# Optimization experiments

Measured on AMD Instinct MI355X. Metric: run time of the kernel, lower is better.

## Reference

```python
import jax, jax.numpy as jnp
import numpy as np

IN_SIZE = 512
UNITS = 512
GRID_SIZE = 5
ORDER = 3
LO, HI = -1.0, 1.0
BATCH = 1024


def _make_grid():
    # grid: (in_size, grid_size + 2*order + 1), extended beyond grid_range by order knot spacings
    bound = HI - LO
    g = jnp.linspace(LO - ORDER * bound / GRID_SIZE,
                     HI + ORDER * bound / GRID_SIZE,
                     GRID_SIZE + 2 * ORDER + 1, dtype=jnp.float32)
    return jnp.tile(g[None, :], (IN_SIZE, 1))


def _spline_bases(x, grid):
    # Cox-de Boor recursion. x: (B, in), grid: (in, G)
    xe = x[..., None]  # (B, in, 1)
    bases = ((xe >= grid[:, :-1]) & (xe < grid[:, 1:])).astype(x.dtype)  # order-0 indicators
    for k in range(1, ORDER + 1):
        left = (xe - grid[:, :-(k + 1)]) / (grid[:, k:-1] - grid[:, :-(k + 1)]) * bases[..., :-1]
        right = (grid[:, k + 1:] - xe) / (grid[:, k + 1:] - grid[:, 1:-k]) * bases[..., 1:]
        bases = left + right
    return bases  # (B, in, grid_size + order)


def setup_inputs() -> dict:
    key = jax.random.key(0)
    k1, k2, k3 = jax.random.split(key, 3)
    x = jax.random.normal(k1, (BATCH, IN_SIZE), jnp.float32)
    spline_kernel = 0.1 * jax.random.normal(k2, (IN_SIZE, GRID_SIZE + ORDER, UNITS), jnp.float32)
    limit = float(np.sqrt(6.0 / (IN_SIZE + UNITS)))  # GlorotUniform
    scale_factor = jax.random.uniform(k3, (IN_SIZE, UNITS), jnp.float32, -limit, limit)
    bias = jnp.zeros((UNITS,), jnp.float32)
    return {"x": x, "spline_kernel": spline_kernel, "scale_factor": scale_factor, "bias": bias}


def reference(x, spline_kernel, scale_factor, bias):
    grid = _make_grid()
    bases = _spline_bases(x, grid)                              # (B, in, basis)
    spline_out = jnp.einsum('bik,iko->bio', bases, spline_kernel)  # (B, in, units)
    spline_out = spline_out + jax.nn.silu(x)[..., None]            # add basis activation per feature
    spline_out = spline_out * scale_factor[None]                   # per (in, units) scaling
    out = jnp.sum(spline_out, axis=-2) + bias                      # reduce over in_size
    return out
```

## Files before the change

kernel.cpp:

```cpp
#include <hip/hip_runtime.h>
#include <cstdint>
#include <cmath>

typedef unsigned short u16;
typedef __bf16 bf16x8 __attribute__((ext_vector_type(8)));
typedef float f32x4 __attribute__((ext_vector_type(4)));

#define B_SZ   1024
#define IN_SZ  512
#define U_SZ   512
#define KTOT   4608
#define SPLITS 16
#define KLEN   288
#define BK     32
#define KITERS 9

__device__ __forceinline__ u16 f2bf(float f) {
  __bf16 h = (__bf16)f;
  return __builtin_bit_cast(u16, h);
}

__device__ __forceinline__ void async16(const void* g, void* l) {
  __builtin_amdgcn_global_load_lds(
      (__attribute__((address_space(1))) void*)(g),
      (__attribute__((address_space(3))) void*)(l), 16u, 0, 0u);
}

__global__ void prep_w(const float* __restrict__ SK, const float* __restrict__ SF,
                       u16* __restrict__ WT) {
  __shared__ u16 tile[72 * 64];
  const int o0 = blockIdx.x * 64;
  const int i0 = blockIdx.y * 8;
  const int tid = threadIdx.x;
  const int oo = tid & 63, grp = tid >> 6;

  for (int tr = grp; tr < 72; tr += 4) {
    int i = i0 + tr / 9;
    int k = tr % 9;
    float sf = SF[(size_t)i * U_SZ + o0 + oo];
    float v  = (k < 8) ? SK[((size_t)i * 8 + k) * U_SZ + o0 + oo] * sf : sf;
    tile[tr * 64 + oo] = f2bf(v);
  }
  __syncthreads();

  const int t0 = i0 * 9;
  for (int idx = tid; idx < 72 * 64; idx += 256) {
    int ol = idx / 72;
    int c  = idx - ol * 72;
    WT[(size_t)(o0 + ol) * KTOT + t0 + c] = tile[c * 64 + ol];
  }
}

__global__ void bases_kernel(const float* __restrict__ X, u16* __restrict__ A) {
  const int gid = blockIdx.x * 256 + threadIdx.x;
  const float x = X[gid];

  const float T0 = -2.2f, H = 0.4f;
  float b0[11], b1[10], b2[9], b3[8];
#pragma unroll
  for (int j = 0; j < 11; ++j) {
    float tj  = T0 + H * j;
    float tj1 = T0 + H * (j + 1);
    b0[j] = (x >= tj && x < tj1) ? 1.0f : 0.0f;
  }
#pragma unroll
  for (int j = 0; j < 10; ++j) {
    float tj  = T0 + H * j;
    float tj2 = T0 + H * (j + 2);
    b1[j] = (x - tj) * 2.5f * b0[j] + (tj2 - x) * 2.5f * b0[j + 1];
  }
#pragma unroll
  for (int j = 0; j < 9; ++j) {
    float tj  = T0 + H * j;
    float tj3 = T0 + H * (j + 3);
    b2[j] = (x - tj) * 1.25f * b1[j] + (tj3 - x) * 1.25f * b1[j + 1];
  }
#pragma unroll
  for (int j = 0; j < 8; ++j) {
    float tj  = T0 + H * j;
    float tj4 = T0 + H * (j + 4);
    b3[j] = (x - tj) * (1.0f / 1.2f) * b2[j] + (tj4 - x) * (1.0f / 1.2f) * b2[j + 1];
  }
  float sil = x / (1.0f + expf(-x));

  u16* row = A + (size_t)gid * 9;
#pragma unroll
  for (int k = 0; k < 8; ++k) row[k] = f2bf(b3[k]);
  row[8] = f2bf(sil);
}

__global__ void __launch_bounds__(256) gemm_kan(const u16* __restrict__ A,
                                                const u16* __restrict__ WT,
                                                float* __restrict__ P) {
  __shared__ __align__(16) u16 sA[2][128 * BK];
  __shared__ __align__(16) u16 sB[2][128 * BK];

  const int t    = threadIdx.x;
  const int lane = t & 63;
  const int w    = t >> 6;
  const int wr   = w >> 1;
  const int wn   = w & 1;
  const int m0   = blockIdx.x * 128;
  const int n0   = blockIdx.y * 128;
  const int kbase = blockIdx.z * KLEN;

  const int srow = t >> 2, sc = t & 3;
  const int sg0 = (sc ^ (srow & 3)) * 8;
  const int srow1 = (t + 256) >> 2, sc1 = t & 3;
  const int sg1 = (sc1 ^ (srow1 & 3)) * 8;
  const u16* gA0 = A  + (size_t)(m0 + srow)  * KTOT + sg0;
  const u16* gA1 = A  + (size_t)(m0 + srow1) * KTOT + sg1;
  const u16* gB0 = WT + (size_t)(n0 + srow)  * KTOT + sg0;
  const u16* gB1 = WT + (size_t)(n0 + srow1) * KTOT + sg1;

  f32x4 acc[4][4];
#pragma unroll
  for (int i = 0; i < 4; ++i)
#pragma unroll
    for (int j = 0; j < 4; ++j) acc[i][j] = (f32x4)0.0f;

  auto stage = [&](int buf, int k0) {
    char* lA = (char*)(&sA[buf][0]) + t * 16;
    char* lB = (char*)(&sB[buf][0]) + t * 16;
    async16(gA0 + k0, lA);
    async16(gA1 + k0, lA + 4096);
    async16(gB0 + k0, lB);
    async16(gB1 + k0, lB + 4096);
  };

  stage(0, kbase);

  const int m = lane & 15, q = lane >> 4;
  const int qs = (q ^ (m & 3)) * 16;
  const char* fA = (const char*)(&sA[0][0]) + (wr * 64 + m) * (BK * 2) + qs;
  const char* fB = (const char*)(&sB[0][0]) + (wn * 64 + m) * (BK * 2) + qs;
  const int bufstep = 128 * BK * 2;

#pragma unroll
  for (int it = 0; it < KITERS; ++it) {
    const int cur = it & 1;
    __syncthreads();
    if (it + 1 < KITERS) stage(cur ^ 1, kbase + (it + 1) * BK);

    bf16x8 af[4], bfv[4];
#pragma unroll
    for (int tt = 0; tt < 4; ++tt)
      af[tt] = *(const bf16x8*)(fA + cur * bufstep + tt * 16 * (BK * 2));
#pragma unroll
    for (int tt = 0; tt < 4; ++tt)
      bfv[tt] = *(const bf16x8*)(fB + cur * bufstep + tt * 16 * (BK * 2));
#pragma unroll
    for (int mt = 0; mt < 4; ++mt)
#pragma unroll
      for (int nt = 0; nt < 4; ++nt)
        acc[mt][nt] = __builtin_amdgcn_mfma_f32_16x16x32_bf16(
            af[mt], bfv[nt], acc[mt][nt], 0, 0, 0);
  }

  float* Pp = P + (size_t)blockIdx.z * (B_SZ * U_SZ);
#pragma unroll
  for (int mt = 0; mt < 4; ++mt)
#pragma unroll
    for (int rr = 0; rr < 4; ++rr) {
      int row = m0 + wr * 64 + mt * 16 + q * 4 + rr;
      size_t rb = (size_t)row * U_SZ + n0 + wn * 64 + m;
#pragma unroll
      for (int nt = 0; nt < 4; ++nt) Pp[rb + nt * 16] = acc[mt][nt][rr];
    }
}

__global__ void reduce_kernel(const float* __restrict__ P,
                              const float* __restrict__ bias,
                              float* __restrict__ out) {
  const int idx = blockIdx.x * 256 + threadIdx.x;
  const f32x4* P4 = (const f32x4*)P;
  f32x4 acc = P4[idx];
#pragma unroll
  for (int s = 1; s < SPLITS; ++s) acc += P4[(size_t)s * (B_SZ * U_SZ / 4) + idx];
  acc += ((const f32x4*)bias)[idx & 127];
  ((f32x4*)out)[idx] = acc;
}

extern "C" void kernel_launch(void* const* d_in, const int* in_sizes, int n_in,
                              void* d_out, int out_size, void* d_ws, size_t ws_size,
                              hipStream_t stream) {
  const float* X    = (const float*)d_in[0];
  const float* SK   = (const float*)d_in[1];
  const float* SF   = (const float*)d_in[2];
  const float* bias = (const float*)d_in[3];

  char* ws = (char*)d_ws;
  u16*   WT = (u16*)ws;
  u16*   A  = (u16*)(ws + 4718592);
  float* P  = (float*)(ws + 4718592 + 9437184);

  hipLaunchKernelGGL(prep_w,        dim3(8, 64),    dim3(256), 0, stream, SK, SF, WT);
  hipLaunchKernelGGL(bases_kernel,  dim3(2048),     dim3(256), 0, stream, X, A);
  hipLaunchKernelGGL(gemm_kan,      dim3(8, 4, 16), dim3(256), 0, stream, A, WT, P);
  hipLaunchKernelGGL(reduce_kernel, dim3(512),      dim3(256), 0, stream, P, bias, (float*)d_out);
}
```

Before: 98.60 us.

## Merge prep kernels and replace split-K partial buffer with atomic accumulation

Combines weight prep, basis computation and bias initialization of the output into a single launch, and has the split-K GEMM add its results straight into the output with float atomics instead of writing 16 partial buffers and running a separate reduction. This removes two kernel launches and the round trip of 32 MB of partial sums. It also pads the transpose tile to cut LDS bank conflicts and stages basis writes through LDS so global stores coalesce. In exchange, summation order becomes nondeterministic and atomic contention on the output is added.

After: 107.5 us. 1.09x slower.

```diff
diff --git a/kernel.cpp b/kernel.cpp
--- a/kernel.cpp
+++ b/kernel.cpp
@@ -26,72 +26,84 @@
       (__attribute__((address_space(3))) void*)(l), 16u, 0, 0u);
 }
 
-__global__ void prep_w(const float* __restrict__ SK, const float* __restrict__ SF,
-                       u16* __restrict__ WT) {
-  __shared__ u16 tile[72 * 64];
-  const int o0 = blockIdx.x * 64;
-  const int i0 = blockIdx.y * 8;
+__global__ void __launch_bounds__(256) prep_all(const float* __restrict__ SK,
+                                                const float* __restrict__ SF,
+                                                const float* __restrict__ X,
+                                                const float* __restrict__ bias,
+                                                u16* __restrict__ WT,
+                                                u16* __restrict__ A,
+                                                float* __restrict__ out) {
+  const int bx = blockIdx.x;
   const int tid = threadIdx.x;
-  const int oo = tid & 63, grp = tid >> 6;
-
-  for (int tr = grp; tr < 72; tr += 4) {
-    int i = i0 + tr / 9;
-    int k = tr % 9;
-    float sf = SF[(size_t)i * U_SZ + o0 + oo];
-    float v  = (k < 8) ? SK[((size_t)i * 8 + k) * U_SZ + o0 + oo] * sf : sf;
-    tile[tr * 64 + oo] = f2bf(v);
+
+  if (bx < 512) {
+    __shared__ u16 tile[72 * 66];
+    const int o0 = (bx & 7) * 64;
+    const int i0 = (bx >> 3) * 8;
+    const int oo = tid & 63, grp = tid >> 6;
+    for (int tr = grp; tr < 72; tr += 4) {
+      int i = i0 + tr / 9;
+      int k = tr % 9;
+      float sf = SF[(size_t)i * U_SZ + o0 + oo];
+      float v  = (k < 8) ? SK[((size_t)i * 8 + k) * U_SZ + o0 + oo] * sf : sf;
+      tile[tr * 66 + oo] = f2bf(v);
+    }
+    __syncthreads();
+    const int t0 = i0 * 9;
+    for (int idx = tid; idx < 72 * 64; idx += 256) {
+      int ol = idx / 72;
+      int c  = idx - ol * 72;
+      WT[(size_t)(o0 + ol) * KTOT + t0 + c] = tile[c * 66 + ol];
+    }
+  } else if (bx < 2560) {
+    __shared__ u16 st[2304];
+    const int gid0 = (bx - 512) * 256;
+    const float x = X[gid0 + tid];
+
+    const float T0 = -2.2f, H = 0.4f;
+    float b0[11], b1[10], b2[9], b3[8];
+#pragma unroll
+    for (int j = 0; j < 11; ++j) {
+      float tj  = T0 + H * j;
+      float tj1 = T0 + H * (j + 1);
+      b0[j] = (x >= tj && x < tj1) ? 1.0f : 0.0f;
+    }
+#pragma unroll
+    for (int j = 0; j < 10; ++j) {
+      float tj  = T0 + H * j;
+      float tj2 = T0 + H * (j + 2);
+      b1[j] = (x - tj) * 2.5f * b0[j] + (tj2 - x) * 2.5f * b0[j + 1];
+    }
+#pragma unroll
+    for (int j = 0; j < 9; ++j) {
+      float tj  = T0 + H * j;
+      float tj3 = T0 + H * (j + 3);
+      b2[j] = (x - tj) * 1.25f * b1[j] + (tj3 - x) * 1.25f * b1[j + 1];
+    }
+#pragma unroll
+    for (int j = 0; j < 8; ++j) {
+      float tj  = T0 + H * j;
+      float tj4 = T0 + H * (j + 4);
+      b3[j] = (x - tj) * (1.0f / 1.2f) * b2[j] + (tj4 - x) * (1.0f / 1.2f) * b2[j + 1];
+    }
+    float sil = x / (1.0f + expf(-x));
+
+#pragma unroll
+    for (int k = 0; k < 8; ++k) st[tid * 9 + k] = f2bf(b3[k]);
+    st[tid * 9 + 8] = f2bf(sil);
+    __syncthreads();
+    u16* dst = A + (size_t)gid0 * 9;
+#pragma unroll
+    for (int j = 0; j < 9; ++j) dst[j * 256 + tid] = st[j * 256 + tid];
+  } else {
+    const int idx = (bx - 2560) * 256 + tid;
+    ((f32x4*)out)[idx] = ((const f32x4*)bias)[idx & 127];
   }
-  __syncthreads();
-
-  const int t0 = i0 * 9;
-  for (int idx = tid; idx < 72 * 64; idx += 256) {
-    int ol = idx / 72;
-    int c  = idx - ol * 72;
-    WT[(size_t)(o0 + ol) * KTOT + t0 + c] = tile[c * 64 + ol];
-  }
-}
-
-__global__ void bases_kernel(const float* __restrict__ X, u16* __restrict__ A) {
-  const int gid = blockIdx.x * 256 + threadIdx.x;
-  const float x = X[gid];
-
-  const float T0 = -2.2f, H = 0.4f;
-  float b0[11], b1[10], b2[9], b3[8];
-#pragma unroll
-  for (int j = 0; j < 11; ++j) {
-    float tj  = T0 + H * j;
-    float tj1 = T0 + H * (j + 1);
-    b0[j] = (x >= tj && x < tj1) ? 1.0f : 0.0f;
-  }
-#pragma unroll
-  for (int j = 0; j < 10; ++j) {
-    float tj  = T0 + H * j;
-    float tj2 = T0 + H * (j + 2);
-    b1[j] = (x - tj) * 2.5f * b0[j] + (tj2 - x) * 2.5f * b0[j + 1];
-  }
-#pragma unroll
-  for (int j = 0; j < 9; ++j) {
-    float tj  = T0 + H * j;
-    float tj3 = T0 + H * (j + 3);
-    b2[j] = (x - tj) * 1.25f * b1[j] + (tj3 - x) * 1.25f * b1[j + 1];
-  }
-#pragma unroll
-  for (int j = 0; j < 8; ++j) {
-    float tj  = T0 + H * j;
-    float tj4 = T0 + H * (j + 4);
-    b3[j] = (x - tj) * (1.0f / 1.2f) * b2[j] + (tj4 - x) * (1.0f / 1.2f) * b2[j + 1];
-  }
-  float sil = x / (1.0f + expf(-x));
-
-  u16* row = A + (size_t)gid * 9;
-#pragma unroll
-  for (int k = 0; k < 8; ++k) row[k] = f2bf(b3[k]);
-  row[8] = f2bf(sil);
 }
 
 __global__ void __launch_bounds__(256) gemm_kan(const u16* __restrict__ A,
                                                 const u16* __restrict__ WT,
-                                                float* __restrict__ P) {
+                                                float* __restrict__ out) {
   __shared__ __align__(16) u16 sA[2][128 * BK];
   __shared__ __align__(16) u16 sB[2][128 * BK];
 
@@ -157,7 +169,6 @@
             af[mt], bfv[nt], acc[mt][nt], 0, 0, 0);
   }
 
-  float* Pp = P + (size_t)blockIdx.z * (B_SZ * U_SZ);
 #pragma unroll
   for (int mt = 0; mt < 4; ++mt)
 #pragma unroll
@@ -165,20 +176,9 @@
       int row = m0 + wr * 64 + mt * 16 + q * 4 + rr;
       size_t rb = (size_t)row * U_SZ + n0 + wn * 64 + m;
 #pragma unroll
-      for (int nt = 0; nt < 4; ++nt) Pp[rb + nt * 16] = acc[mt][nt][rr];
-    }
-}
-
-__global__ void reduce_kernel(const float* __restrict__ P,
-                              const float* __restrict__ bias,
-                              float* __restrict__ out) {
-  const int idx = blockIdx.x * 256 + threadIdx.x;
-  const f32x4* P4 = (const f32x4*)P;
-  f32x4 acc = P4[idx];
-#pragma unroll
-  for (int s = 1; s < SPLITS; ++s) acc += P4[(size_t)s * (B_SZ * U_SZ / 4) + idx];
-  acc += ((const f32x4*)bias)[idx & 127];
-  ((f32x4*)out)[idx] = acc;
+      for (int nt = 0; nt < 4; ++nt)
+        unsafeAtomicAdd(&out[rb + nt * 16], acc[mt][nt][rr]);
+    }
 }
 
 extern "C" void kernel_launch(void* const* d_in, const int* in_sizes, int n_in,
@@ -190,12 +190,11 @@
   const float* bias = (const float*)d_in[3];
 
   char* ws = (char*)d_ws;
-  u16*   WT = (u16*)ws;
-  u16*   A  = (u16*)(ws + 4718592);
-  float* P  = (float*)(ws + 4718592 + 9437184);
-
-  hipLaunchKernelGGL(prep_w,        dim3(8, 64),    dim3(256), 0, stream, SK, SF, WT);
-  hipLaunchKernelGGL(bases_kernel,  dim3(2048),     dim3(256), 0, stream, X, A);
-  hipLaunchKernelGGL(gemm_kan,      dim3(8, 4, 16), dim3(256), 0, stream, A, WT, P);
-  hipLaunchKernelGGL(reduce_kernel, dim3(512),      dim3(256), 0, stream, P, bias, (float*)d_out);
-}
+  u16* WT = (u16*)ws;
+  u16* A  = (u16*)(ws + 4718592);
+  float* out = (float*)d_out;
+
+  hipLaunchKernelGGL(prep_all, dim3(3072),     dim3(256), 0, stream,
+                     SK, SF, X, bias, WT, A, out);
+  hipLaunchKernelGGL(gemm_kan, dim3(8, 4, 16), dim3(256), 0, stream, A, WT, out);
+}
```
